# Kernel optimization log

Hardware: AMD Instinct MI355X
Metric: run time of the kernel (lower is better)

## Reference

```python
import jax, jax.numpy as jnp
import numpy as np

IN_DIM = 512
RATIO = 8
QK_DIM = IN_DIM // RATIO  # 64
B, C, H, W = 8, IN_DIM, 64, 64


def setup_inputs() -> dict:
    key = jax.random.key(0)
    ks = jax.random.split(key, 9)
    x = jax.random.normal(ks[0], (B, C, H, W), dtype=jnp.float32)
    y = jax.random.normal(ks[1], (B, C, H, W), dtype=jnp.float32)
    z = jax.random.normal(ks[2], (B, C, H, W), dtype=jnp.float32)
    # 1x1 conv weights, xavier_normal with gain=0.02: std = gain*sqrt(2/(fan_in+fan_out))
    def xavier(k, out_c, in_c, gain=0.02):
        std = gain * np.sqrt(2.0 / (in_c + out_c))
        return jax.random.normal(k, (out_c, in_c), dtype=jnp.float32) * std
    Wq = xavier(ks[3], QK_DIM, C)
    Wk = xavier(ks[4], QK_DIM, C)
    Wv = xavier(ks[5], C, C)
    bq = jnp.zeros((QK_DIM,), dtype=jnp.float32)
    bk = jnp.zeros((QK_DIM,), dtype=jnp.float32)
    bv = jnp.zeros((C,), dtype=jnp.float32)
    gamma = jnp.zeros((1,), dtype=jnp.float32)
    return {"x": x, "y": y, "z": z, "Wq": Wq, "bq": bq, "Wk": Wk,
            "bk": bk, "Wv": Wv, "bv": bv, "gamma": gamma}


def reference(x, y, z, Wq, bq, Wk, bk, Wv, bv, gamma):
    b, c, h, w = x.shape
    n = h * w
    # 1x1 convs == per-pixel linear projections
    q = (jnp.einsum('oc,bchw->bohw', Wq, x) + bq[None, :, None, None]).reshape(b, -1, n)  # [B, d, N]
    k = (jnp.einsum('oc,bchw->bohw', Wk, y) + bk[None, :, None, None]).reshape(b, -1, n)  # [B, d, N]
    v = (jnp.einsum('oc,bchw->bohw', Wv, z) + bv[None, :, None, None]).reshape(b, -1, n)  # [B, C, N]
    # energy[b, i, j] = <q[:, i], k[:, j]>, no scaling (matches original)
    energy = jnp.einsum('bdn,bdm->bnm', q, k)      # [B, N, N]
    attention = jax.nn.softmax(energy, axis=-1)     # softmax over keys
    # out = value @ attention^T : out[:, c, i] = sum_j v[:, c, j] * attention[:, i, j]
    out = jnp.einsum('bcj,bij->bci', v, attention)  # [B, C, N]
    out = out.reshape(b, c, h, w)
    out = gamma[0] * out + x
    return out
```

## Files before the change

### kernel.cpp

```cpp
#include <hip/hip_runtime.h>
#include <hip/hip_bf16.h>
#include <hip/hip_fp8.h>
#include <stdint.h>

#define B_   8
#define C_   512
#define NPIX 4096
#define VLDB 4160

typedef __attribute__((ext_vector_type(8))) short bf16x8;
typedef __attribute__((ext_vector_type(4))) float f32x4;

__device__ __forceinline__ uint16_t f2bf(float f) {
    union { float f; uint32_t u; } v; v.f = f;
    uint32_t u = v.u;
    return (uint16_t)((u + 0x7FFFu + ((u >> 16) & 1u)) >> 16);
}

__device__ __forceinline__ uint32_t pk2(float a, float b) {
    union { __hip_bfloat162 h; uint32_t u; } c;
    c.h = __float22bfloat162_rn(make_float2(a, b));
    return c.u;
}

__device__ __forceinline__ float fexp2(float x) {
#if __has_builtin(__builtin_amdgcn_exp2f)
    return __builtin_amdgcn_exp2f(x);
#else
    return exp2f(x);
#endif
}

template<bool HI>
__device__ __forceinline__ uint32_t pk_fp8(float a, float b, uint32_t old) {
#if __has_builtin(__builtin_amdgcn_cvt_pk_fp8_f32)
    return __builtin_amdgcn_cvt_pk_fp8_f32(a, b, old, HI);
#else
    union { __hip_fp8_storage_t s[4]; uint32_t u; } r; r.u = old;
    r.s[HI * 2 + 0] = __hip_cvt_float_to_fp8(a, __HIP_SATFINITE, __HIP_E4M3);
    r.s[HI * 2 + 1] = __hip_cvt_float_to_fp8(b, __HIP_SATFINITE, __HIP_E4M3);
    return r.u;
#endif
}
__device__ __forceinline__ uint8_t f2fp8(float a) {
#if __has_builtin(__builtin_amdgcn_cvt_pk_fp8_f32)
    uint32_t u = __builtin_amdgcn_cvt_pk_fp8_f32(a, 0.f, 0u, false);
    return (uint8_t)(u & 0xFF);
#else
    return __hip_cvt_float_to_fp8(a, __HIP_SATFINITE, __HIP_E4M3);
#endif
}

__global__ __launch_bounds__(256, 2) void proj_kernel(
    const float* __restrict__ X, const float* __restrict__ W,
    const float* __restrict__ bias, uint16_t* __restrict__ out,
    float scale)
{
    __shared__ char xt[64 * 128];
    const int b  = blockIdx.z;
    const int n0 = blockIdx.x * 64;
    const int t = threadIdx.x, w = t >> 6, l = t & 63;
    const int l15 = l & 15, lg = l >> 4;
    const float* Xb = X + (size_t)b * C_ * NPIX + n0;

    f32x4 acc[4] = {};

    for (int cc = 0; cc < C_; cc += 64) {
        __syncthreads();
        #pragma unroll
        for (int i = 0; i < 16; i += 2) {
            int c = w * 16 + i;
            float f0 = Xb[(size_t)(cc + c) * NPIX + l];
            float f1 = Xb[(size_t)(cc + c + 1) * NPIX + l];
            uint32_t pair = pk2(f0, f1);
            int byte = (l * 128 + c * 2) ^ ((l & 7) << 4);
            *(uint32_t*)(xt + byte) = pair;
        }
        __syncthreads();
        #pragma unroll
        for (int kk = 0; kk < 2; kk++) {
            int o  = w * 16 + l15;
            int cb = cc + kk * 32 + lg * 8;
            float4 wa = *(const float4*)&W[(size_t)o * C_ + cb];
            float4 wb = *(const float4*)&W[(size_t)o * C_ + cb + 4];
            union { bf16x8 v; uint32_t u[4]; } afu;
            afu.u[0] = pk2(wa.x, wa.y); afu.u[1] = pk2(wa.z, wa.w);
            afu.u[2] = pk2(wb.x, wb.y); afu.u[3] = pk2(wb.z, wb.w);
            #pragma unroll
            for (int jt = 0; jt < 4; jt++) {
                int n = jt * 16 + l15;
                int byte = (n * 128 + (kk * 32 + lg * 8) * 2) ^ ((n & 7) << 4);
                bf16x8 bfr = *(bf16x8*)(xt + byte);
                acc[jt] = __builtin_amdgcn_mfma_f32_16x16x32_bf16(afu.v, bfr, acc[jt], 0, 0, 0);
            }
        }
    }
    int og = w * 16 + lg * 4;
    #pragma unroll
    for (int jt = 0; jt < 4; jt++) {
        int n = n0 + jt * 16 + l15;
        #pragma unroll
        for (int r = 0; r < 4; r++) {
            float v = (acc[jt][r] + bias[og + r]) * scale;
            out[((size_t)b * NPIX + n) * 64 + og + r] = f2bf(v);
        }
    }
}

__global__ __launch_bounds__(256, 2) void projv_kernel(
    const float* __restrict__ X, const float* __restrict__ W,
    const float* __restrict__ bias, uint8_t* __restrict__ outp)
{
    __shared__ char xt[64 * 1024];
    const int b  = blockIdx.z;
    const int n0 = blockIdx.x * 64;
    const int t = threadIdx.x, w = t >> 6, l = t & 63;
    const int l15 = l & 15, lg = l >> 4;
    const float* Xb = X + (size_t)b * C_ * NPIX + n0;

    for (int cc = 0; cc < C_; cc += 64) {
        #pragma unroll
        for (int i = 0; i < 16; i += 2) {
            int c = cc + w * 16 + i;
            float f0 = Xb[(size_t)c * NPIX + l];
            float f1 = Xb[(size_t)(c + 1) * NPIX + l];
            uint32_t pair = pk2(f0, f1);
            int byte = (l * 1024 + c * 2) ^ ((l & 7) << 4);
            *(uint32_t*)(xt + byte) = pair;
        }
    }
    __syncthreads();

    #pragma unroll 1
    for (int o0 = 0; o0 < C_; o0 += 64) {
        f32x4 acc[4] = {};
        #pragma unroll 1
        for (int cc = 0; cc < C_; cc += 64) {
            #pragma unroll
            for (int kk = 0; kk < 2; kk++) {
                int o  = o0 + w * 16 + l15;
                int cb = cc + kk * 32 + lg * 8;
                float4 wa = *(const float4*)&W[(size_t)o * C_ + cb];
                float4 wb = *(const float4*)&W[(size_t)o * C_ + cb + 4];
                union { bf16x8 v; uint32_t u[4]; } afu;
                afu.u[0] = pk2(wa.x, wa.y); afu.u[1] = pk2(wa.z, wa.w);
                afu.u[2] = pk2(wb.x, wb.y); afu.u[3] = pk2(wb.z, wb.w);
                #pragma unroll
                for (int jt = 0; jt < 4; jt++) {
                    int n = jt * 16 + l15;
                    int byte = (n * 1024 + cb * 2) ^ ((n & 7) << 4);
                    bf16x8 bfr = *(bf16x8*)(xt + byte);
                    acc[jt] = __builtin_amdgcn_mfma_f32_16x16x32_bf16(afu.v, bfr, acc[jt], 0, 0, 0);
                }
            }
        }
        int og = o0 + w * 16 + lg * 4;
        #pragma unroll
        for (int jt = 0; jt < 4; jt++) {
            int j6 = jt * 16 + l15;
            int pos = ((j6 >> 3) & 3) * 16 + ((j6 >> 5) << 3) + (j6 & 7);
            #pragma unroll
            for (int r = 0; r < 4; r++) {
                float v = (acc[jt][r] + bias[og + r]) * 64.0f;
                outp[((size_t)b * C_ + og + r) * (size_t)VLDB + (size_t)(n0 >> 6) * 64 + pos] = f2fp8(v);
            }
        }
    }
}

__global__ __launch_bounds__(256, 2) void attn_kernel(
    const uint16_t* __restrict__ qT, const uint16_t* __restrict__ kT,
    const uint8_t* __restrict__ vB, const float* __restrict__ X,
    const float* __restrict__ gamma_p, float* __restrict__ out)
{
    __shared__ char  Pl[3][64 * 64];
    __shared__ float lsum[64][5];

    const int id  = blockIdx.x;
    const int xcd = id & 7, slot = id >> 3;
    const int g   = xcd + 8 * (slot >> 6);
    const int qt  = slot & 63;
    const int b   = g >> 1, cb = g & 1;
    const int i0  = qt * 64;

    const int t = threadIdx.x, w = t >> 6, l = t & 63;
    const int l15 = l & 15, lg = l >> 4;
    const int c0 = cb * 256 + w * 64;

    auto barrier_lds = [&]() {
        asm volatile("s_waitcnt lgkmcnt(0)" ::: "memory");
        __builtin_amdgcn_s_barrier();
    };

    bf16x8 q8[4][2];
    #pragma unroll
    for (int it = 0; it < 4; it++)
        #pragma unroll
        for (int kk = 0; kk < 2; kk++)
            q8[it][kk] = *(const bf16x8*)&qT[((size_t)b * NPIX + i0 + it*16 + l15) * 64 + kk*32 + lg*8];

    f32x4 oacc[4][4] = {};
    float l_part[4] = {0.f, 0.f, 0.f, 0.f};

    const uint16_t* kTb = kT + (size_t)b * NPIX * 64;
    const uint8_t*  vBb = vB + ((size_t)b * C_ + c0) * (size_t)VLDB + lg * 16;
    const uint16_t* kROW = kTb + (size_t)(w * 16 + l15) * 64 + lg * 8;

    int vrowB[4];
    #pragma unroll
    for (int ct = 0; ct < 4; ct++) vrowB[ct] = (ct * 16 + l15) * VLDB;

    bf16x8 k8[2];
    ulong2 vreg[4];
    f32x4 s[4];

    auto loadK = [&](int step) {
        const uint16_t* p = kROW + (size_t)step * (64 * 64);
        k8[0] = *(const bf16x8*)p;
        k8[1] = *(const bf16x8*)(p + 32);
    };
    auto loadV = [&](int step) {
        const uint8_t* p = vBb + (size_t)step * 64;
        #pragma unroll
        for (int ct = 0; ct < 4; ct++)
            vreg[ct] = *(const ulong2*)(p + vrowB[ct]);
    };
    auto QK = [&]() {
        #pragma unroll
        for (int it = 0; it < 4; it++) s[it] = f32x4{0.f, 0.f, 0.f, 0.f};
        __builtin_amdgcn_s_setprio(1);
        #pragma unroll
        for (int kk = 0; kk < 2; kk++)
            #pragma unroll
            for (int it = 0; it < 4; it++)
                s[it] = __builtin_amdgcn_mfma_f32_16x16x32_bf16(k8[kk], q8[it][kk], s[it], 0, 0, 0);
        __builtin_amdgcn_s_setprio(0);
    };
    auto PcomputeWrite = [&](char* Pn) {
        #pragma unroll
        for (int it = 0; it < 4; it++) {
            float e0 = fexp2(fminf(s[it][0], 60.f));
            float e1 = fexp2(fminf(s[it][1], 60.f));
            float e2 = fexp2(fminf(s[it][2], 60.f));
            float e3 = fexp2(fminf(s[it][3], 60.f));
            l_part[it] += (e0 + e1) + (e2 + e3);
            uint32_t p4 = pk_fp8<false>(e0, e1, 0u);
            p4 = pk_fp8<true>(e2, e3, p4);
            int i = it * 16 + l15;
            int byte = (i * 64 + w * 16 + lg * 4) ^ ((i & 7) << 3);
            *(uint32_t*)(Pn + byte) = p4;
        }
    };
    auto PV = [&](const char* P) {
        __builtin_amdgcn_s_setprio(1);
        #pragma unroll
        for (int kk = 0; kk < 2; kk++) {
            long pb[4];
            #pragma unroll
            for (int it = 0; it < 4; it++) {
                int i = it * 16 + l15;
                int byte = (i * 64 + kk * 32 + lg * 8) ^ ((i & 7) << 3);
                pb[it] = *(const long*)(P + byte);
            }
            #pragma unroll
            for (int ct = 0; ct < 4; ct++) {
                long v8 = (long)(kk ? vreg[ct].y : vreg[ct].x);
                #pragma unroll
                for (int it = 0; it < 4; it++)
                    oacc[ct][it] = __builtin_amdgcn_mfma_f32_16x16x32_fp8_fp8(v8, pb[it], oacc[ct][it], 0, 0, 0);
            }
        }
        __builtin_amdgcn_s_setprio(0);
    };

    loadK(0);
    loadV(0);
    QK();
    loadK(1);
    PcomputeWrite(Pl[0]);
    QK();
    loadK(2);
    PcomputeWrite(Pl[1]);

    char* Pprev = Pl[0];
    char* Pcur  = Pl[1];
    char* Pnext = Pl[2];

    #pragma unroll 1
    for (int jt_ = 1; jt_ < 64; ++jt_) {
        barrier_lds();
        PV(Pprev);
        loadV(jt_);
        if (jt_ < 63) {
            QK();
            if (jt_ < 62) loadK(jt_ + 2);
            PcomputeWrite(Pnext);
        }
        char* tmp = Pprev; Pprev = Pcur; Pcur = Pnext; Pnext = tmp;
    }
    barrier_lds();
    PV(Pprev);

    #pragma unroll
    for (int it = 0; it < 4; it++) {
        float v = l_part[it];
        v += __shfl_xor(v, 16);
        v += __shfl_xor(v, 32);
        if (lg == 0) lsum[it * 16 + l15][w] = v;
    }
    __syncthreads();

    float gamma = gamma_p[0];
    float rl[4];
    #pragma unroll
    for (int it = 0; it < 4; it++) {
        int i = it * 16 + l15;
        rl[it] = 1.0f / (64.0f * ((lsum[i][0] + lsum[i][1]) + (lsum[i][2] + lsum[i][3])));
    }
    #pragma unroll
    for (int ct = 0; ct < 4; ct++)
        #pragma unroll
        for (int r = 0; r < 4; r++) {
            int c = c0 + ct * 16 + lg * 4 + r;
            #pragma unroll
            for (int it = 0; it < 4; it++) {
                int n = i0 + it * 16 + l15;
                size_t idx = ((size_t)b * C_ + c) * NPIX + n;
                out[idx] = gamma * (oacc[ct][it][r] * rl[it]) + X[idx];
            }
        }
}

extern "C" void kernel_launch(void* const* d_in, const int* in_sizes, int n_in,
                              void* d_out, int out_size, void* d_ws, size_t ws_size,
                              hipStream_t stream) {
    const float* x     = (const float*)d_in[0];
    const float* y     = (const float*)d_in[1];
    const float* z     = (const float*)d_in[2];
    const float* Wq    = (const float*)d_in[3];
    const float* bq    = (const float*)d_in[4];
    const float* Wk    = (const float*)d_in[5];
    const float* bk    = (const float*)d_in[6];
    const float* Wv    = (const float*)d_in[7];
    const float* bv    = (const float*)d_in[8];
    const float* gamma = (const float*)d_in[9];
    float* out = (float*)d_out;

    uint16_t* qT = (uint16_t*)d_ws;
    uint16_t* kT = qT + (size_t)B_ * NPIX * 64;
    uint8_t*  vb = (uint8_t*)(kT + (size_t)B_ * NPIX * 64);

    proj_kernel <<<dim3(64, 1, 8), dim3(256), 0, stream>>>(x, Wq, bq, qT, 1.4426950408889634f);
    proj_kernel <<<dim3(64, 1, 8), dim3(256), 0, stream>>>(y, Wk, bk, kT, 1.0f);
    projv_kernel<<<dim3(64, 1, 8), dim3(256), 0, stream>>>(z, Wv, bv, vb);
    attn_kernel <<<dim3(1024), dim3(256), 0, stream>>>(qT, kT, vb, x, gamma, out);
}
```

Baseline: 266.0 us.

## Quantize Q/K to fp8 and restructure attention into 512-thread blocks with LDS-staged V

Q and K projections are now stored as scaled fp8 (scales 16*log2e and 16, undone by a 1/256 factor before exp2), so QK^T runs on fp8 MFMA with half the K/Q bytes. The attention kernel moves to 512-thread blocks covering 128 queries by 256 channels. V tiles are cooperatively staged into double-buffered swizzled LDS and shared by two query groups, instead of each wave loading V directly from global memory. This aims to cut K/V global traffic and QK cost, at the price of fp8 precision loss in the logits and lower occupancy (one block per CU).

```diff
diff --git a/kernel.cpp b/kernel.cpp
--- a/kernel.cpp
+++ b/kernel.cpp
@@ -10,12 +10,6 @@
 
 typedef __attribute__((ext_vector_type(8))) short bf16x8;
 typedef __attribute__((ext_vector_type(4))) float f32x4;
-
-__device__ __forceinline__ uint16_t f2bf(float f) {
-    union { float f; uint32_t u; } v; v.f = f;
-    uint32_t u = v.u;
-    return (uint16_t)((u + 0x7FFFu + ((u >> 16) & 1u)) >> 16);
-}
 
 __device__ __forceinline__ uint32_t pk2(float a, float b) {
     union { __hip_bfloat162 h; uint32_t u; } c;
@@ -51,9 +45,13 @@
 #endif
 }
 
-__global__ __launch_bounds__(256, 2) void proj_kernel(
+__device__ __forceinline__ int perm64(int d) {
+    return ((d >> 3) & 3) * 16 + ((d >> 5) << 3) + (d & 7);
+}
+
+__global__ __launch_bounds__(256, 2) void projqk_kernel(
     const float* __restrict__ X, const float* __restrict__ W,
-    const float* __restrict__ bias, uint16_t* __restrict__ out,
+    const float* __restrict__ bias, uint8_t* __restrict__ outp,
     float scale)
 {
     __shared__ char xt[64 * 128];
@@ -102,7 +100,7 @@
         #pragma unroll
         for (int r = 0; r < 4; r++) {
             float v = (acc[jt][r] + bias[og + r]) * scale;
-            out[((size_t)b * NPIX + n) * 64 + og + r] = f2bf(v);
+            outp[((size_t)b * NPIX + n) * 64 + perm64(og + r)] = f2fp8(v);
         }
     }
 }
@@ -158,7 +156,7 @@
         #pragma unroll
         for (int jt = 0; jt < 4; jt++) {
             int j6 = jt * 16 + l15;
-            int pos = ((j6 >> 3) & 3) * 16 + ((j6 >> 5) << 3) + (j6 & 7);
+            int pos = perm64(j6);
             #pragma unroll
             for (int r = 0; r < 4; r++) {
                 float v = (acc[jt][r] + bias[og + r]) * 64.0f;
@@ -168,103 +166,113 @@
     }
 }
 
-__global__ __launch_bounds__(256, 2) void attn_kernel(
-    const uint16_t* __restrict__ qT, const uint16_t* __restrict__ kT,
+__global__ __launch_bounds__(512, 1) void attn_kernel(
+    const uint8_t* __restrict__ qT, const uint8_t* __restrict__ kT,
     const uint8_t* __restrict__ vB, const float* __restrict__ X,
     const float* __restrict__ gamma_p, float* __restrict__ out)
 {
-    __shared__ char  Pl[3][64 * 64];
-    __shared__ float lsum[64][5];
-
-    const int id  = blockIdx.x;
-    const int xcd = id & 7, slot = id >> 3;
-    const int g   = xcd + 8 * (slot >> 6);
-    const int qt  = slot & 63;
-    const int b   = g >> 1, cb = g & 1;
-    const int i0  = qt * 64;
+    __shared__ char  Pl[3][128 * 64];
+    __shared__ char  Vl[2][16384];
+    __shared__ float lsum[128][5];
+
+    const int id = blockIdx.x;
+    const int b  = id & 7;
+    const int rr = id >> 3;
+    const int qt = rr & 31, cb = rr >> 5;
+    const int i0 = qt * 128;
 
     const int t = threadIdx.x, w = t >> 6, l = t & 63;
+    const int iq = w >> 2, cq = w & 3;
     const int l15 = l & 15, lg = l >> 4;
-    const int c0 = cb * 256 + w * 64;
 
     auto barrier_lds = [&]() {
         asm volatile("s_waitcnt lgkmcnt(0)" ::: "memory");
         __builtin_amdgcn_s_barrier();
     };
 
-    bf16x8 q8[4][2];
-    #pragma unroll
-    for (int it = 0; it < 4; it++)
-        #pragma unroll
-        for (int kk = 0; kk < 2; kk++)
-            q8[it][kk] = *(const bf16x8*)&qT[((size_t)b * NPIX + i0 + it*16 + l15) * 64 + kk*32 + lg*8];
+    ulong2 qf[4];
+    {
+        const uint8_t* qbase = qT + ((size_t)b * NPIX + i0 + iq * 64) * 64;
+        #pragma unroll
+        for (int it = 0; it < 4; it++)
+            qf[it] = *(const ulong2*)(qbase + (it * 16 + l15) * 64 + lg * 16);
+    }
 
     f32x4 oacc[4][4] = {};
     float l_part[4] = {0.f, 0.f, 0.f, 0.f};
 
-    const uint16_t* kTb = kT + (size_t)b * NPIX * 64;
-    const uint8_t*  vBb = vB + ((size_t)b * C_ + c0) * (size_t)VLDB + lg * 16;
-    const uint16_t* kROW = kTb + (size_t)(w * 16 + l15) * 64 + lg * 8;
-
-    int vrowB[4];
-    #pragma unroll
-    for (int ct = 0; ct < 4; ct++) vrowB[ct] = (ct * 16 + l15) * VLDB;
-
-    bf16x8 k8[2];
-    ulong2 vreg[4];
+    const uint8_t* kROW = kT + (size_t)b * NPIX * 64 + (size_t)(cq * 16 + l15) * 64 + lg * 16;
+    const uint8_t* vblk = vB + ((size_t)b * C_ + cb * 256) * (size_t)VLDB;
+
+    const int g0 = t, g1 = 512 + t;
+    const int row0 = g0 >> 2, cq0 = g0 & 3;
+    const int row1 = g1 >> 2, cq1 = g1 & 3;
+    const uint8_t* vsrc0 = vblk + (size_t)row0 * VLDB + cq0 * 16;
+    const uint8_t* vsrc1 = vblk + (size_t)row1 * VLDB + cq1 * 16;
+    const int vdst0 = row0 * 64 + ((cq0 ^ (row0 & 3)) * 16);
+    const int vdst1 = row1 * 64 + ((cq1 ^ (row1 & 3)) * 16);
+
+    ulong2 kv, vt0, vt1;
     f32x4 s[4];
 
     auto loadK = [&](int step) {
-        const uint16_t* p = kROW + (size_t)step * (64 * 64);
-        k8[0] = *(const bf16x8*)p;
-        k8[1] = *(const bf16x8*)(p + 32);
-    };
-    auto loadV = [&](int step) {
-        const uint8_t* p = vBb + (size_t)step * 64;
-        #pragma unroll
-        for (int ct = 0; ct < 4; ct++)
-            vreg[ct] = *(const ulong2*)(p + vrowB[ct]);
+        kv = *(const ulong2*)(kROW + (size_t)step * 4096);
+    };
+    auto vstage_load = [&](int step) {
+        vt0 = *(const ulong2*)(vsrc0 + (size_t)step * 64);
+        vt1 = *(const ulong2*)(vsrc1 + (size_t)step * 64);
+    };
+    auto vstage_write = [&](int buf) {
+        *(ulong2*)(Vl[buf] + vdst0) = vt0;
+        *(ulong2*)(Vl[buf] + vdst1) = vt1;
     };
     auto QK = [&]() {
         #pragma unroll
         for (int it = 0; it < 4; it++) s[it] = f32x4{0.f, 0.f, 0.f, 0.f};
         __builtin_amdgcn_s_setprio(1);
         #pragma unroll
-        for (int kk = 0; kk < 2; kk++)
-            #pragma unroll
-            for (int it = 0; it < 4; it++)
-                s[it] = __builtin_amdgcn_mfma_f32_16x16x32_bf16(k8[kk], q8[it][kk], s[it], 0, 0, 0);
+        for (int it = 0; it < 4; it++)
+            s[it] = __builtin_amdgcn_mfma_f32_16x16x32_fp8_fp8((long)kv.x, (long)qf[it].x, s[it], 0, 0, 0);
+        #pragma unroll
+        for (int it = 0; it < 4; it++)
+            s[it] = __builtin_amdgcn_mfma_f32_16x16x32_fp8_fp8((long)kv.y, (long)qf[it].y, s[it], 0, 0, 0);
         __builtin_amdgcn_s_setprio(0);
     };
     auto PcomputeWrite = [&](char* Pn) {
         #pragma unroll
         for (int it = 0; it < 4; it++) {
-            float e0 = fexp2(fminf(s[it][0], 60.f));
-            float e1 = fexp2(fminf(s[it][1], 60.f));
-            float e2 = fexp2(fminf(s[it][2], 60.f));
-            float e3 = fexp2(fminf(s[it][3], 60.f));
+            float e0 = fexp2(fminf(s[it][0] * 0.00390625f, 60.f));
+            float e1 = fexp2(fminf(s[it][1] * 0.00390625f, 60.f));
+            float e2 = fexp2(fminf(s[it][2] * 0.00390625f, 60.f));
+            float e3 = fexp2(fminf(s[it][3] * 0.00390625f, 60.f));
             l_part[it] += (e0 + e1) + (e2 + e3);
             uint32_t p4 = pk_fp8<false>(e0, e1, 0u);
             p4 = pk_fp8<true>(e2, e3, p4);
-            int i = it * 16 + l15;
-            int byte = (i * 64 + w * 16 + lg * 4) ^ ((i & 7) << 3);
+            int i = iq * 64 + it * 16 + l15;
+            int byte = (i * 64 + cq * 16 + lg * 4) ^ ((i & 7) << 3);
             *(uint32_t*)(Pn + byte) = p4;
         }
     };
-    auto PV = [&](const char* P) {
+    auto PV = [&](const char* P, const char* V) {
         __builtin_amdgcn_s_setprio(1);
+        ulong2 vf[4];
+        #pragma unroll
+        for (int ct = 0; ct < 4; ct++) {
+            int row = cq * 64 + ct * 16 + l15;
+            vf[ct] = *(const ulong2*)(V + row * 64 + ((lg ^ (row & 3)) * 16));
+        }
         #pragma unroll
         for (int kk = 0; kk < 2; kk++) {
             long pb[4];
             #pragma unroll
             for (int it = 0; it < 4; it++) {
-                int i = it * 16 + l15;
+                int i = iq * 64 + it * 16 + l15;
                 int byte = (i * 64 + kk * 32 + lg * 8) ^ ((i & 7) << 3);
                 pb[it] = *(const long*)(P + byte);
             }
             #pragma unroll
             for (int ct = 0; ct < 4; ct++) {
-                long v8 = (long)(kk ? vreg[ct].y : vreg[ct].x);
+                long v8 = (long)(kk ? vf[ct].y : vf[ct].x);
                 #pragma unroll
                 for (int it = 0; it < 4; it++)
                     oacc[ct][it] = __builtin_amdgcn_mfma_f32_16x16x32_fp8_fp8(v8, pb[it], oacc[ct][it], 0, 0, 0);
@@ -274,10 +282,12 @@
     };
 
     loadK(0);
-    loadV(0);
+    vstage_load(0);
     QK();
     loadK(1);
     PcomputeWrite(Pl[0]);
+    vstage_write(0);
+    vstage_load(1);
     QK();
     loadK(2);
     PcomputeWrite(Pl[1]);
@@ -289,9 +299,10 @@
     #pragma unroll 1
     for (int jt_ = 1; jt_ < 64; ++jt_) {
         barrier_lds();
-        PV(Pprev);
-        loadV(jt_);
+        PV(Pprev, Vl[(jt_ - 1) & 1]);
+        vstage_write(jt_ & 1);
         if (jt_ < 63) {
+            vstage_load(jt_ + 1);
             QK();
             if (jt_ < 62) loadK(jt_ + 2);
             PcomputeWrite(Pnext);
@@ -299,14 +310,14 @@
         char* tmp = Pprev; Pprev = Pcur; Pcur = Pnext; Pnext = tmp;
     }
     barrier_lds();
-    PV(Pprev);
+    PV(Pprev, Vl[1]);
 
     #pragma unroll
     for (int it = 0; it < 4; it++) {
         float v = l_part[it];
         v += __shfl_xor(v, 16);
         v += __shfl_xor(v, 32);
-        if (lg == 0) lsum[it * 16 + l15][w] = v;
+        if (lg == 0) lsum[iq * 64 + it * 16 + l15][cq] = v;
     }
     __syncthreads();
 
@@ -314,17 +325,17 @@
     float rl[4];
     #pragma unroll
     for (int it = 0; it < 4; it++) {
-        int i = it * 16 + l15;
+        int i = iq * 64 + it * 16 + l15;
         rl[it] = 1.0f / (64.0f * ((lsum[i][0] + lsum[i][1]) + (lsum[i][2] + lsum[i][3])));
     }
     #pragma unroll
     for (int ct = 0; ct < 4; ct++)
         #pragma unroll
         for (int r = 0; r < 4; r++) {
-            int c = c0 + ct * 16 + lg * 4 + r;
+            int c = cb * 256 + cq * 64 + ct * 16 + lg * 4 + r;
             #pragma unroll
             for (int it = 0; it < 4; it++) {
-                int n = i0 + it * 16 + l15;
+                int n = i0 + iq * 64 + it * 16 + l15;
                 size_t idx = ((size_t)b * C_ + c) * NPIX + n;
                 out[idx] = gamma * (oacc[ct][it][r] * rl[it]) + X[idx];
             }
@@ -346,12 +357,12 @@
     const float* gamma = (const float*)d_in[9];
     float* out = (float*)d_out;
 
-    uint16_t* qT = (uint16_t*)d_ws;
-    uint16_t* kT = qT + (size_t)B_ * NPIX * 64;
-    uint8_t*  vb = (uint8_t*)(kT + (size_t)B_ * NPIX * 64);
-
-    proj_kernel <<<dim3(64, 1, 8), dim3(256), 0, stream>>>(x, Wq, bq, qT, 1.4426950408889634f);
-    proj_kernel <<<dim3(64, 1, 8), dim3(256), 0, stream>>>(y, Wk, bk, kT, 1.0f);
-    projv_kernel<<<dim3(64, 1, 8), dim3(256), 0, stream>>>(z, Wv, bv, vb);
-    attn_kernel <<<dim3(1024), dim3(256), 0, stream>>>(qT, kT, vb, x, gamma, out);
-}
+    uint8_t* qT = (uint8_t*)d_ws;
+    uint8_t* kT = qT + (size_t)B_ * NPIX * 64;
+    uint8_t* vb = kT + (size_t)B_ * NPIX * 64;
+
+    projqk_kernel<<<dim3(64, 1, 8), dim3(256), 0, stream>>>(x, Wq, bq, qT, 23.083120654223414f);
+    projqk_kernel<<<dim3(64, 1, 8), dim3(256), 0, stream>>>(y, Wk, bk, kT, 16.0f);
+    projv_kernel <<<dim3(64, 1, 8), dim3(256), 0, stream>>>(z, Wv, bv, vb);
+    attn_kernel  <<<dim3(512), dim3(512), 0, stream>>>(qT, kT, vb, x, gamma, out);
+}
```

Result: slower. 277.0 us (+4.1%).
